# Performance work log

Hardware: AMD Instinct MI355X
Metric: run time of the kernel (lower is better)

## Reference

```python
import jax, jax.numpy as jnp
import numpy as np

HIDDEN = 256
HEADS = 8
HEAD_DIM = HIDDEN // HEADS  # 32
N_NODES = 50000
N_EDGES = 800000


def setup_inputs() -> dict:
    key = jax.random.key(0)
    ks = jax.random.split(key, 12)
    h = jax.random.normal(ks[0], (N_NODES, HIDDEN), dtype=jnp.float32)
    row = jax.random.randint(ks[1], (N_EDGES,), 0, N_NODES, dtype=jnp.int64 if jax.config.jax_enable_x64 else jnp.int32)
    col = jax.random.randint(ks[2], (N_EDGES,), 0, N_NODES, dtype=jnp.int64 if jax.config.jax_enable_x64 else jnp.int32)
    def lin(kw, kb):
        W = jax.random.normal(kw, (HIDDEN, HIDDEN), dtype=jnp.float32) * 0.02
        b = jax.random.normal(kb, (HIDDEN,), dtype=jnp.float32) * 0.02
        return W, b
    Wq, bq = lin(ks[3], ks[4])
    Wk, bk = lin(ks[5], ks[6])
    Wv, bv = lin(ks[7], ks[8])
    Wo, bo = lin(ks[9], ks[10])
    return {"h": h, "row": row, "col": col,
            "Wq": Wq, "bq": bq, "Wk": Wk, "bk": bk,
            "Wv": Wv, "bv": bv, "Wo": Wo, "bo": bo}


def reference(h, row, col, Wq, bq, Wk, bk, Wv, bv, Wo, bo):
    N = h.shape[0]
    scaling = HEAD_DIM ** (-0.5)
    # torch Linear: x @ W.T + b; reshape to (N, head_dim, num_heads) as in source
    q = (h @ Wq.T + bq).reshape(N, HEAD_DIM, HEADS) * scaling
    k = (h @ Wk.T + bk).reshape(N, HEAD_DIM, HEADS)
    v = (h @ Wv.T + bv).reshape(N, HEAD_DIM, HEADS)
    # SDDMM: per-edge, per-head score = q[row] . k[col]   -> [E, H]
    s = jnp.einsum('edh,edh->eh', q[row], k[col])
    # sparse softmax over nonzeros of each row
    m = jax.ops.segment_max(s, row, num_segments=N)          # [N, H]
    e = jnp.exp(s - m[row])                                   # [E, H]
    z = jax.ops.segment_sum(e, row, num_segments=N)          # [N, H]
    attn = e / z[row]                                         # [E, H]
    # SPMM: out[i] = sum over edges (i,j) attn[e,h] * v[j,:,h]
    out = jax.ops.segment_sum(attn[:, None, :] * v[col], row, num_segments=N)  # [N, D, H]
    return out.reshape(N, -1) @ Wo.T + bo
```

## Files before the change

### kernel.cpp

```cpp
#include <hip/hip_runtime.h>
#include <hip/hip_bf16.h>
#include <math.h>

#define N_NODES  50000
#define N_EDGES  800000
#define HIDDEN   256
#define HEADS    8
#define HEAD_DIM 32
#define MAXDEG   64
#define KVSTRIDE 512
#define MTILES   391

using short8 = __attribute__((ext_vector_type(8))) short;
using f32x4  = __attribute__((ext_vector_type(4))) float;

__device__ __forceinline__ float b2f(unsigned short u) {
  union { unsigned int i; float f; } v; v.i = ((unsigned int)u) << 16; return v.f;
}
__device__ __forceinline__ unsigned short f2b(float f) {
  union { float f; unsigned int i; } v; v.f = f;
  unsigned int r = v.i + 0x7FFF + ((v.i >> 16) & 1);
  return (unsigned short)(r >> 16);
}
__device__ __forceinline__ void unpack2(unsigned int d, float& lo, float& hi) {
  union { unsigned int i; float f; } a, b;
  a.i = d << 16; b.i = d & 0xFFFF0000u;
  lo = a.f; hi = b.f;
}

__global__ __launch_bounds__(256) void detect(const unsigned short* __restrict__ h16,
                                              const int* __restrict__ rowraw,
                                              int* __restrict__ flags) {
  __shared__ int nan_cnt, hi_viol, lo_pos;
  const int tid = threadIdx.x;
  if (tid == 0) { nan_cnt = 0; hi_viol = 0; lo_pos = 0; }
  __syncthreads();
  int local = 0;
  for (int i = tid; i < 16384; i += 256)
    if ((h16[i] & 0x7F80) == 0x7F80) local++;
  if (local) atomicAdd(&nan_cnt, local);
  int viol = 0, pos = 0;
  for (int e = tid; e < 512; e += 256) {
    if (rowraw[2 * e + 1] != 0) viol++;
    if (rowraw[2 * e] > 0) pos++;
  }
  if (viol) atomicAdd(&hi_viol, viol);
  if (pos) atomicAdd(&lo_pos, pos);
  __syncthreads();
  if (tid == 0) {
    flags[0] = (nan_cnt >= 4) ? 1 : 0;
    flags[1] = (hi_viol == 0 && lo_pos > 0) ? 1 : 0;
  }
}

__global__ __launch_bounds__(256) void conv_f4(const void* __restrict__ src,
                                               unsigned short* __restrict__ dst, int n4,
                                               const int* __restrict__ flags) {
  const int fp32 = flags[0];
  for (int i = blockIdx.x * 256 + threadIdx.x; i < n4; i += gridDim.x * 256) {
    if (fp32) {
      const float4 v = ((const float4*)src)[i];
      ushort4 o; o.x = f2b(v.x); o.y = f2b(v.y); o.z = f2b(v.z); o.w = f2b(v.w);
      ((ushort4*)dst)[i] = o;
    } else {
      ((ushort4*)dst)[i] = ((const ushort4*)src)[i];
    }
  }
}

struct WPtrs {
  const void* srcW[4]; unsigned short* dstW[4];
  const void* srcB[4]; unsigned short* dstB[4];
};
__global__ __launch_bounds__(256) void conv_wb(WPtrs p, const int* __restrict__ flags) {
  const int fp32 = flags[0];
  const int idx = blockIdx.x * 256 + threadIdx.x;
  if (idx < 49152) {
    const int m = idx >> 14, r = idx & 16383;
    const int g = r >> 6, kc = r & 63;
    const int f = ((g & 31) << 3) | (g >> 5);
    const int s = f * 64 + kc;
    if (fp32) {
      const float4 v = ((const float4*)p.srcW[m])[s];
      ushort4 o; o.x = f2b(v.x); o.y = f2b(v.y); o.z = f2b(v.z); o.w = f2b(v.w);
      ((ushort4*)p.dstW[m])[g * 64 + kc] = o;
    } else {
      ((ushort4*)p.dstW[m])[g * 64 + kc] = ((const ushort4*)p.srcW[m])[s];
    }
  } else if (idx < 49152 + 65536) {
    const int g = idx - 49152;
    const int f = g >> 8, kk = g & 255;
    const int s = f * 256 + (((kk & 31) << 3) | (kk >> 5));
    p.dstW[3][g] = fp32 ? f2b(((const float*)p.srcW[3])[s])
                        : ((const unsigned short*)p.srcW[3])[s];
  } else if (idx < 49152 + 65536 + 256) {
    const int t = idx - 49152 - 65536;
    const int m = t >> 6, r = t & 63;
    if (m < 3) {
      ushort4 o;
      #pragma unroll
      for (int x = 0; x < 4; ++x) {
        const int g = r * 4 + x;
        const int f = ((g & 31) << 3) | (g >> 5);
        ((unsigned short*)&o)[x] = fp32 ? f2b(((const float*)p.srcB[m])[f])
                                        : ((const unsigned short*)p.srcB[m])[f];
      }
      ((ushort4*)p.dstB[m])[r] = o;
    } else {
      if (fp32) {
        const float4 v = ((const float4*)p.srcB[3])[r];
        ushort4 o; o.x = f2b(v.x); o.y = f2b(v.y); o.z = f2b(v.z); o.w = f2b(v.w);
        ((ushort4*)p.dstB[3])[r] = o;
      } else {
        ((ushort4*)p.dstB[3])[r] = ((const ushort4*)p.srcB[3])[r];
      }
    }
  }
}

__global__ __launch_bounds__(256) void build_buckets(
    const int* __restrict__ rowraw, const int* __restrict__ colraw,
    const int* __restrict__ flags, int* __restrict__ cursor, int* __restrict__ bucket)
{
  const int e = blockIdx.x * 256 + threadIdx.x;
  if (e >= N_EDGES) return;
  const int i64 = flags[1];
  const int r = i64 ? rowraw[2 * e] : rowraw[e];
  const int c = i64 ? colraw[2 * e] : colraw[e];
  const int pos = atomicAdd(&cursor[r], 1);
  if (pos < MAXDEG) bucket[r * MAXDEG + pos] = c;
}

#if defined(__has_builtin)
#if __has_builtin(__builtin_amdgcn_global_load_lds)
#define HAVE_GLL 1
#endif
#endif
__device__ __forceinline__ void stage_tile(
    const unsigned short* __restrict__ src, int row_base, int row_max,
    int kb, unsigned short* lds, int wave, int lane)
{
  #pragma unroll
  for (int c = 0; c < 4; ++c) {
    const int chunk = wave * 4 + c;
    const int r = chunk * 8 + (lane >> 3);
    int gr = row_base + r; if (gr > row_max) gr = row_max;
    const int scb = (lane & 7) ^ ((lane >> 3) & 7);
    const unsigned short* gp = src + (size_t)gr * HIDDEN + kb * 64 + scb * 8;
#ifdef HAVE_GLL
    __builtin_amdgcn_global_load_lds(
        (const __attribute__((address_space(1))) void*)gp,
        (__attribute__((address_space(3))) void*)(lds + chunk * 512),
        16, 0, 0);
#else
    *(short8*)(lds + chunk * 512 + lane * 8) = *(const short8*)gp;
#endif
  }
}

#define GEMM_CORE(A_SRC, AROWB, AROWM, B_SRC, BROWB, BROWM)                          \
  __shared__ unsigned short sA[8192], sB[8192];                                      \
  const int wave = threadIdx.x >> 6, lane = threadIdx.x & 63;                        \
  const int lrow = lane & 15, quad = lane >> 4;                                      \
  const int wr0 = (wave & 1) * 64, wc0 = (wave >> 1) * 64;                           \
  f32x4 acc[4][4];                                                                   \
  _Pragma("unroll")                                                                  \
  for (int i = 0; i < 4; ++i)                                                        \
    _Pragma("unroll")                                                                \
    for (int j = 0; j < 4; ++j) acc[i][j] = (f32x4){0.f, 0.f, 0.f, 0.f};            \
  for (int kb = 0; kb < 4; ++kb) {                                                   \
    if (kb) __syncthreads();                                                         \
    stage_tile(A_SRC, AROWB, AROWM, kb, sA, wave, lane);                             \
    stage_tile(B_SRC, BROWB, BROWM, kb, sB, wave, lane);                             \
    __syncthreads();                                                                 \
    _Pragma("unroll")                                                                \
    for (int kk = 0; kk < 2; ++kk) {                                                 \
      short8 af[4], bf[4];                                                           \
      _Pragma("unroll")                                                              \
      for (int i = 0; i < 4; ++i) {                                                  \
        const int rr = wr0 + i * 16 + lrow;                                          \
        af[i] = *(const short8*)(sA + rr * 64 + (((kk * 4 + quad) ^ (lrow & 7)) * 8));\
      }                                                                              \
      _Pragma("unroll")                                                              \
      for (int j = 0; j < 4; ++j) {                                                  \
        const int rr = wc0 + j * 16 + lrow;                                          \
        bf[j] = *(const short8*)(sB + rr * 64 + (((kk * 4 + quad) ^ (lrow & 7)) * 8));\
      }                                                                              \
      _Pragma("unroll")                                                              \
      for (int i = 0; i < 4; ++i)                                                    \
        _Pragma("unroll")                                                            \
        for (int j = 0; j < 4; ++j)                                                  \
          acc[i][j] = __builtin_amdgcn_mfma_f32_16x16x32_bf16(af[i], bf[j], acc[i][j], 0, 0, 0); \
    }                                                                                \
  }

__global__ __launch_bounds__(256) void gemm_qkv(
    const unsigned short* __restrict__ X, const unsigned short* __restrict__ WQKV,
    const unsigned short* __restrict__ biasAll,
    unsigned short* __restrict__ Qt, unsigned short* __restrict__ KV, float qscale)
{
  const int row0 = blockIdx.x * 128;
  const int col0 = blockIdx.y * 128;
  GEMM_CORE(X, row0, N_NODES - 1, WQKV, col0, 767)

  #pragma unroll
  for (int j = 0; j < 4; ++j) {
    const int gcol = col0 + wc0 + j * 16;
    const int m = gcol >> 8;
    const int f = (gcol & 255) + lrow;
    const float scale = (m == 0) ? qscale : 1.0f;
    const float bv = b2f(biasAll[gcol + lrow]);
    unsigned short* bp = (m == 0) ? Qt : (KV + ((m == 2) ? 256 : 0));
    const int ldv = (m == 0) ? 256 : KVSTRIDE;
    #pragma unroll
    for (int i = 0; i < 4; ++i) {
      #pragma unroll
      for (int r = 0; r < 4; ++r) {
        const int row = row0 + wr0 + i * 16 + quad * 4 + r;
        if (row < N_NODES)
          bp[(size_t)row * ldv + f] = f2b((acc[i][j][r] + bv) * scale);
      }
    }
  }
}

__global__ __launch_bounds__(256) void gemm_o(
    const unsigned short* __restrict__ X, const unsigned short* __restrict__ W,
    const unsigned short* __restrict__ bias, void* __restrict__ Yv,
    const int* __restrict__ flags)
{
  const int row0 = blockIdx.x * 128;
  const int col0 = blockIdx.y * 128;
  const int out_fp32 = flags[0];
  GEMM_CORE(X, row0, N_NODES - 1, W, col0, 255)

  #pragma unroll
  for (int j = 0; j < 4; ++j) {
    const int col = col0 + wc0 + j * 16 + lrow;
    const float bv = b2f(bias[col]);
    #pragma unroll
    for (int i = 0; i < 4; ++i) {
      #pragma unroll
      for (int r = 0; r < 4; ++r) {
        const int row = row0 + wr0 + i * 16 + quad * 4 + r;
        if (row < N_NODES) {
          const float y = acc[i][j][r] + bv;
          if (out_fp32) ((float*)Yv)[(size_t)row * HIDDEN + col] = y;
          else ((unsigned short*)Yv)[(size_t)row * HIDDEN + col] = f2b(y);
        }
      }
    }
  }
}

__global__ __launch_bounds__(256) void attn_fused(
    const unsigned short* __restrict__ Qt, const unsigned short* __restrict__ KV,
    const int* __restrict__ cursor, const int* __restrict__ bucket,
    unsigned short* __restrict__ pre)
{
  const int node = blockIdx.x * 4 + (threadIdx.x >> 6);
  if (node >= N_NODES) return;
  const int lane = threadIdx.x & 63;
  const int side = lane >> 5;
  const int sub  = lane & 31;
  const unsigned suboff = (unsigned)(sub * 8);
  int cnt = cursor[node]; if (cnt > MAXDEG) cnt = MAXDEG;

  const uint4 qd = *(const uint4*)(Qt + (unsigned)node * HIDDEN + suboff);
  float q[8];
  unpack2(qd.x, q[0], q[1]); unpack2(qd.y, q[2], q[3]);
  unpack2(qd.z, q[4], q[5]); unpack2(qd.w, q[6], q[7]);

  float a[8] = {0.f, 0.f, 0.f, 0.f, 0.f, 0.f, 0.f, 0.f};
  float z = 0.f;

  if (cnt > 0) {
    const int last = cnt - 1;
    const int* brow = bucket + node * MAXDEG;
    const int myidx = brow[lane <= last ? lane : last];
    const int nit = (cnt + 1) >> 1;

    auto compute = [&](const uint4& kk, const uint4& vv, int jj) {
      float kf[8];
      unpack2(kk.x, kf[0], kf[1]); unpack2(kk.y, kf[2], kf[3]);
      unpack2(kk.z, kf[4], kf[5]); unpack2(kk.w, kf[6], kf[7]);
      float s0 = q[0]*kf[0] + q[2]*kf[2] + q[4]*kf[4] + q[6]*kf[6];
      float s1 = q[1]*kf[1] + q[3]*kf[3] + q[5]*kf[5] + q[7]*kf[7];
      float d = s0 + s1;
      d += __shfl_xor(d, 1, 64);
      d += __shfl_xor(d, 2, 64);
      float w = __expf(d);
      if (2 * jj + side > last) w = 0.f;
      z += w;
      float vf[8];
      unpack2(vv.x, vf[0], vf[1]); unpack2(vv.y, vf[2], vf[3]);
      unpack2(vv.z, vf[4], vf[5]); unpack2(vv.w, vf[6], vf[7]);
      #pragma unroll
      for (int x = 0; x < 8; ++x) a[x] = fmaf(w, vf[x], a[x]);
    };

    const int cA = __shfl(myidx, side, 64);
    const unsigned offA = ((unsigned)cA << 9) + suboff;
    uint4 kA = *(const uint4*)(KV + offA);
    uint4 vA = *(const uint4*)(KV + offA + 256u);

    const int cB = __shfl(myidx, 2 + side, 64);
    const unsigned offB = ((unsigned)cB << 9) + suboff;
    uint4 kB = *(const uint4*)(KV + offB);
    uint4 vB = *(const uint4*)(KV + offB + 256u);

    int slC = 4 + side;
    int cC = __shfl(myidx, slC, 64);

    int j = 0;
    #pragma unroll 2
    for (; j + 2 < nit; ++j) {
      const unsigned offC = ((unsigned)cC << 9) + suboff;
      const uint4 kC = *(const uint4*)(KV + offC);
      const uint4 vC = *(const uint4*)(KV + offC + 256u);
      int sl = 2 * (j + 3) + side; if (sl > 63) sl = 63;
      cC = __shfl(myidx, sl, 64);
      compute(kA, vA, j);
      kA = kB; vA = vB; kB = kC; vB = vC;
    }
    compute(kA, vA, j);
    if (j + 1 < nit) compute(kB, vB, j + 1);
  }

  #pragma unroll
  for (int x = 0; x < 8; ++x) a[x] += __shfl_xor(a[x], 32, 64);
  z += __shfl_xor(z, 32, 64);
  const float zi = (z > 0.f) ? (1.f / z) : 0.f;

  if (side == 0) {
    short8 ov;
    #pragma unroll
    for (int x = 0; x < 8; ++x) ov[x] = (short)f2b(a[x] * zi);
    *(short8*)(pre + (unsigned)node * HIDDEN + suboff) = ov;
  }
}

extern "C" void kernel_launch(void* const* d_in, const int* in_sizes, int n_in,
                              void* d_out, int out_size, void* d_ws, size_t ws_size,
                              hipStream_t stream) {
  const void* h_raw  = d_in[0];
  const int* row_raw = (const int*)d_in[1];
  const int* col_raw = (const int*)d_in[2];
  const void* Wq_raw = d_in[3]; const void* bq_raw = d_in[4];
  const void* Wk_raw = d_in[5]; const void* bk_raw = d_in[6];
  const void* Wv_raw = d_in[7]; const void* bv_raw = d_in[8];
  const void* Wo_raw = d_in[9]; const void* bo_raw = d_in[10];

  char* ws = (char*)d_ws;
  unsigned short* Qt   = (unsigned short*)(ws +          0);
  unsigned short* KV   = (unsigned short*)(ws +  25600000);
  int*            cur  = (int*)           (ws +  76800000);
  int*            bkt  = (int*)           (ws +  77000000);
  unsigned short* pre  = (unsigned short*)(ws +  89800000);
  unsigned short* WqP  = (unsigned short*)(ws + 115400000);
  unsigned short* WkP  = WqP + 65536;
  unsigned short* WvP  = WkP + 65536;
  unsigned short* WoP  = WvP + 65536;
  unsigned short* bqP  = (unsigned short*)(ws + 116000000);
  unsigned short* bkP  = bqP + 256;
  unsigned short* bvP  = bkP + 256;
  unsigned short* boC  = bvP + 256;
  int*            flags = (int*)(ws + 116100000);
  unsigned short* Hc   = (unsigned short*)(ws + 117000000);

  hipMemsetAsync(cur, 0, (size_t)N_NODES * 4, stream);

  detect<<<1, 256, 0, stream>>>((const unsigned short*)h_raw, row_raw, flags);

  conv_f4<<<6400, 256, 0, stream>>>(h_raw, Hc, N_NODES * HIDDEN / 4, flags);

  WPtrs wp;
  wp.srcW[0] = Wq_raw; wp.srcW[1] = Wk_raw; wp.srcW[2] = Wv_raw; wp.srcW[3] = Wo_raw;
  wp.dstW[0] = WqP;    wp.dstW[1] = WkP;    wp.dstW[2] = WvP;    wp.dstW[3] = WoP;
  wp.srcB[0] = bq_raw; wp.srcB[1] = bk_raw; wp.srcB[2] = bv_raw; wp.srcB[3] = bo_raw;
  wp.dstB[0] = bqP;    wp.dstB[1] = bkP;    wp.dstB[2] = bvP;    wp.dstB[3] = boC;
  conv_wb<<<(114944 + 255) / 256, 256, 0, stream>>>(wp, flags);

  build_buckets<<<(N_EDGES + 255) / 256, 256, 0, stream>>>(row_raw, col_raw, flags, cur, bkt);

  dim3 qgrid(MTILES, 6);
  gemm_qkv<<<qgrid, 256, 0, stream>>>(Hc, WqP, bqP, Qt, KV, 0.17677669529663687f);

  attn_fused<<<(N_NODES + 3) / 4, 256, 0, stream>>>(Qt, KV, cur, bkt, pre);

  dim3 ogrid(MTILES, 2);
  gemm_o<<<ogrid, 256, 0, stream>>>(pre, WoP, boC, d_out, flags);
}
```

Measured before the change: 393.4 us.

## Merge prep kernels, remap GEMM blocks per XCD, store bucket indices as u16

Merges the memset, detect, h conversion, weight conversion and bucket build into two launches (init and prep), which cuts launch count and inter-kernel gaps. Bucket column indices are stored as 16-bit values, halving bucket traffic in attn_fused. GEMM grids are flattened and remapped so consecutive tiles land on the same XCD, aiming for better L2 reuse of weight and activation tiles. The 16-bit indices assume node ids fit in 16 bits, but N_NODES is 50000, which still fits within 65535.

```diff
diff --git a/kernel.cpp b/kernel.cpp
--- a/kernel.cpp
+++ b/kernel.cpp
@@ -9,7 +9,8 @@
 #define HEAD_DIM 32
 #define MAXDEG   64
 #define KVSTRIDE 512
-#define MTILES   391
+#define QKV_NB   2346
+#define O_NB     782
 
 using short8 = __attribute__((ext_vector_type(8))) short;
 using f32x4  = __attribute__((ext_vector_type(4))) float;
@@ -28,43 +29,42 @@
   lo = a.f; hi = b.f;
 }
 
-__global__ __launch_bounds__(256) void detect(const unsigned short* __restrict__ h16,
-                                              const int* __restrict__ rowraw,
-                                              int* __restrict__ flags) {
-  __shared__ int nan_cnt, hi_viol, lo_pos;
+template<int NB, int NCT>
+__device__ __forceinline__ void xcd_map(int b, int& rt, int& ct) {
+  constexpr int q = NB / 8, r = NB % 8;
+  const int xcd = b & 7, j = b >> 3;
+  const int id = (xcd < r ? xcd * (q + 1) : r * (q + 1) + (xcd - r) * q) + j;
+  rt = id / NCT; ct = id - rt * NCT;
+}
+
+__global__ __launch_bounds__(256) void init(const unsigned short* __restrict__ h16,
+                                            const int* __restrict__ rowraw,
+                                            int* __restrict__ flags,
+                                            int* __restrict__ cur) {
   const int tid = threadIdx.x;
-  if (tid == 0) { nan_cnt = 0; hi_viol = 0; lo_pos = 0; }
-  __syncthreads();
-  int local = 0;
-  for (int i = tid; i < 16384; i += 256)
-    if ((h16[i] & 0x7F80) == 0x7F80) local++;
-  if (local) atomicAdd(&nan_cnt, local);
-  int viol = 0, pos = 0;
-  for (int e = tid; e < 512; e += 256) {
-    if (rowraw[2 * e + 1] != 0) viol++;
-    if (rowraw[2 * e] > 0) pos++;
-  }
-  if (viol) atomicAdd(&hi_viol, viol);
-  if (pos) atomicAdd(&lo_pos, pos);
-  __syncthreads();
-  if (tid == 0) {
-    flags[0] = (nan_cnt >= 4) ? 1 : 0;
-    flags[1] = (hi_viol == 0 && lo_pos > 0) ? 1 : 0;
-  }
-}
-
-__global__ __launch_bounds__(256) void conv_f4(const void* __restrict__ src,
-                                               unsigned short* __restrict__ dst, int n4,
-                                               const int* __restrict__ flags) {
-  const int fp32 = flags[0];
-  for (int i = blockIdx.x * 256 + threadIdx.x; i < n4; i += gridDim.x * 256) {
-    if (fp32) {
-      const float4 v = ((const float4*)src)[i];
-      ushort4 o; o.x = f2b(v.x); o.y = f2b(v.y); o.z = f2b(v.z); o.w = f2b(v.w);
-      ((ushort4*)dst)[i] = o;
-    } else {
-      ((ushort4*)dst)[i] = ((const ushort4*)src)[i];
-    }
+  if (blockIdx.x == 0) {
+    __shared__ int nan_cnt, hi_viol, lo_pos;
+    if (tid == 0) { nan_cnt = 0; hi_viol = 0; lo_pos = 0; }
+    __syncthreads();
+    int local = 0;
+    for (int i = tid; i < 16384; i += 256)
+      if ((h16[i] & 0x7F80) == 0x7F80) local++;
+    if (local) atomicAdd(&nan_cnt, local);
+    int viol = 0, pos = 0;
+    for (int e = tid; e < 512; e += 256) {
+      if (rowraw[2 * e + 1] != 0) viol++;
+      if (rowraw[2 * e] > 0) pos++;
+    }
+    if (viol) atomicAdd(&hi_viol, viol);
+    if (pos) atomicAdd(&lo_pos, pos);
+    __syncthreads();
+    if (tid == 0) {
+      flags[0] = (nan_cnt >= 4) ? 1 : 0;
+      flags[1] = (hi_viol == 0 && lo_pos > 0) ? 1 : 0;
+    }
+  } else {
+    const int i = (blockIdx.x - 1) * 256 + tid;
+    if (i < N_NODES / 4) ((int4*)cur)[i] = make_int4(0, 0, 0, 0);
   }
 }
 
@@ -72,63 +72,80 @@
   const void* srcW[4]; unsigned short* dstW[4];
   const void* srcB[4]; unsigned short* dstB[4];
 };
-__global__ __launch_bounds__(256) void conv_wb(WPtrs p, const int* __restrict__ flags) {
+
+__global__ __launch_bounds__(256) void prep(
+    const void* __restrict__ hsrc, unsigned short* __restrict__ Hc, WPtrs p,
+    const int* __restrict__ rowraw, const int* __restrict__ colraw,
+    const int* __restrict__ flags, int* __restrict__ cursor,
+    unsigned short* __restrict__ bucket)
+{
   const int fp32 = flags[0];
-  const int idx = blockIdx.x * 256 + threadIdx.x;
-  if (idx < 49152) {
-    const int m = idx >> 14, r = idx & 16383;
-    const int g = r >> 6, kc = r & 63;
-    const int f = ((g & 31) << 3) | (g >> 5);
-    const int s = f * 64 + kc;
-    if (fp32) {
-      const float4 v = ((const float4*)p.srcW[m])[s];
-      ushort4 o; o.x = f2b(v.x); o.y = f2b(v.y); o.z = f2b(v.z); o.w = f2b(v.w);
-      ((ushort4*)p.dstW[m])[g * 64 + kc] = o;
-    } else {
-      ((ushort4*)p.dstW[m])[g * 64 + kc] = ((const ushort4*)p.srcW[m])[s];
-    }
-  } else if (idx < 49152 + 65536) {
-    const int g = idx - 49152;
-    const int f = g >> 8, kk = g & 255;
-    const int s = f * 256 + (((kk & 31) << 3) | (kk >> 5));
-    p.dstW[3][g] = fp32 ? f2b(((const float*)p.srcW[3])[s])
-                        : ((const unsigned short*)p.srcW[3])[s];
-  } else if (idx < 49152 + 65536 + 256) {
-    const int t = idx - 49152 - 65536;
-    const int m = t >> 6, r = t & 63;
-    if (m < 3) {
-      ushort4 o;
-      #pragma unroll
-      for (int x = 0; x < 4; ++x) {
-        const int g = r * 4 + x;
-        const int f = ((g & 31) << 3) | (g >> 5);
-        ((unsigned short*)&o)[x] = fp32 ? f2b(((const float*)p.srcB[m])[f])
-                                        : ((const unsigned short*)p.srcB[m])[f];
+  const int bid = blockIdx.x, tid = threadIdx.x;
+
+  if (bid < 6400) {
+    const int n4 = N_NODES * HIDDEN / 4;
+    for (int i = bid * 256 + tid; i < n4; i += 6400 * 256) {
+      if (fp32) {
+        const float4 v = ((const float4*)hsrc)[i];
+        ushort4 o; o.x = f2b(v.x); o.y = f2b(v.y); o.z = f2b(v.z); o.w = f2b(v.w);
+        ((ushort4*)Hc)[i] = o;
+      } else {
+        ((ushort4*)Hc)[i] = ((const ushort4*)hsrc)[i];
       }
-      ((ushort4*)p.dstB[m])[r] = o;
-    } else {
+    }
+  } else if (bid < 6850) {
+    const int idx = (bid - 6400) * 256 + tid;
+    if (idx < 49152) {
+      const int m = idx >> 14, r = idx & 16383;
+      const int g = r >> 6, kc = r & 63;
+      const int f = ((g & 31) << 3) | (g >> 5);
+      const int s = f * 64 + kc;
       if (fp32) {
-        const float4 v = ((const float4*)p.srcB[3])[r];
+        const float4 v = ((const float4*)p.srcW[m])[s];
         ushort4 o; o.x = f2b(v.x); o.y = f2b(v.y); o.z = f2b(v.z); o.w = f2b(v.w);
-        ((ushort4*)p.dstB[3])[r] = o;
+        ((ushort4*)p.dstW[m])[g * 64 + kc] = o;
       } else {
-        ((ushort4*)p.dstB[3])[r] = ((const ushort4*)p.srcB[3])[r];
+        ((ushort4*)p.dstW[m])[g * 64 + kc] = ((const ushort4*)p.srcW[m])[s];
       }
-    }
-  }
-}
-
-__global__ __launch_bounds__(256) void build_buckets(
-    const int* __restrict__ rowraw, const int* __restrict__ colraw,
-    const int* __restrict__ flags, int* __restrict__ cursor, int* __restrict__ bucket)
-{
-  const int e = blockIdx.x * 256 + threadIdx.x;
-  if (e >= N_EDGES) return;
-  const int i64 = flags[1];
-  const int r = i64 ? rowraw[2 * e] : rowraw[e];
-  const int c = i64 ? colraw[2 * e] : colraw[e];
-  const int pos = atomicAdd(&cursor[r], 1);
-  if (pos < MAXDEG) bucket[r * MAXDEG + pos] = c;
+    } else if (idx < 49152 + 65536) {
+      const int g = idx - 49152;
+      const int f = g >> 8, kk = g & 255;
+      const int s = f * 256 + (((kk & 31) << 3) | (kk >> 5));
+      p.dstW[3][g] = fp32 ? f2b(((const float*)p.srcW[3])[s])
+                          : ((const unsigned short*)p.srcW[3])[s];
+    } else if (idx < 49152 + 65536 + 256) {
+      const int t = idx - 49152 - 65536;
+      const int m = t >> 6, r = t & 63;
+      if (m < 3) {
+        ushort4 o;
+        #pragma unroll
+        for (int x = 0; x < 4; ++x) {
+          const int g = r * 4 + x;
+          const int f = ((g & 31) << 3) | (g >> 5);
+          ((unsigned short*)&o)[x] = fp32 ? f2b(((const float*)p.srcB[m])[f])
+                                          : ((const unsigned short*)p.srcB[m])[f];
+        }
+        ((ushort4*)p.dstB[m])[r] = o;
+      } else {
+        if (fp32) {
+          const float4 v = ((const float4*)p.srcB[3])[r];
+          ushort4 o; o.x = f2b(v.x); o.y = f2b(v.y); o.z = f2b(v.z); o.w = f2b(v.w);
+          ((ushort4*)p.dstB[3])[r] = o;
+        } else {
+          ((ushort4*)p.dstB[3])[r] = ((const ushort4*)p.srcB[3])[r];
+        }
+      }
+    }
+  } else {
+    const int e = (bid - 6850) * 256 + tid;
+    if (e < N_EDGES) {
+      const int i64 = flags[1];
+      const int r = i64 ? rowraw[2 * e] : rowraw[e];
+      const int c = i64 ? colraw[2 * e] : colraw[e];
+      const int pos = atomicAdd(&cursor[r], 1);
+      if (pos < MAXDEG) bucket[r * MAXDEG + pos] = (unsigned short)c;
+    }
+  }
 }
 
 #if defined(__has_builtin)
@@ -199,8 +216,9 @@
     const unsigned short* __restrict__ biasAll,
     unsigned short* __restrict__ Qt, unsigned short* __restrict__ KV, float qscale)
 {
-  const int row0 = blockIdx.x * 128;
-  const int col0 = blockIdx.y * 128;
+  int rt, ct; xcd_map<QKV_NB, 6>(blockIdx.x, rt, ct);
+  const int row0 = rt * 128;
+  const int col0 = ct * 128;
   GEMM_CORE(X, row0, N_NODES - 1, WQKV, col0, 767)
 
   #pragma unroll
@@ -229,8 +247,9 @@
     const unsigned short* __restrict__ bias, void* __restrict__ Yv,
     const int* __restrict__ flags)
 {
-  const int row0 = blockIdx.x * 128;
-  const int col0 = blockIdx.y * 128;
+  int rt, ct; xcd_map<O_NB, 2>(blockIdx.x, rt, ct);
+  const int row0 = rt * 128;
+  const int col0 = ct * 128;
   const int out_fp32 = flags[0];
   GEMM_CORE(X, row0, N_NODES - 1, W, col0, 255)
 
@@ -255,7 +274,7 @@
 
 __global__ __launch_bounds__(256) void attn_fused(
     const unsigned short* __restrict__ Qt, const unsigned short* __restrict__ KV,
-    const int* __restrict__ cursor, const int* __restrict__ bucket,
+    const int* __restrict__ cursor, const unsigned short* __restrict__ bucket,
     unsigned short* __restrict__ pre)
 {
   const int node = blockIdx.x * 4 + (threadIdx.x >> 6);
@@ -276,8 +295,8 @@
 
   if (cnt > 0) {
     const int last = cnt - 1;
-    const int* brow = bucket + node * MAXDEG;
-    const int myidx = brow[lane <= last ? lane : last];
+    const unsigned short* brow = bucket + node * MAXDEG;
+    const int myidx = (int)brow[lane <= last ? lane : last];
     const int nit = (cnt + 1) >> 1;
 
     auto compute = [&](const uint4& kk, const uint4& vv, int jj) {
@@ -355,7 +374,7 @@
   unsigned short* Qt   = (unsigned short*)(ws +          0);
   unsigned short* KV   = (unsigned short*)(ws +  25600000);
   int*            cur  = (int*)           (ws +  76800000);
-  int*            bkt  = (int*)           (ws +  77000000);
+  unsigned short* bkt  = (unsigned short*)(ws +  77000000);
   unsigned short* pre  = (unsigned short*)(ws +  89800000);
   unsigned short* WqP  = (unsigned short*)(ws + 115400000);
   unsigned short* WkP  = WqP + 65536;
@@ -368,26 +387,18 @@
   int*            flags = (int*)(ws + 116100000);
   unsigned short* Hc   = (unsigned short*)(ws + 117000000);
 
-  hipMemsetAsync(cur, 0, (size_t)N_NODES * 4, stream);
-
-  detect<<<1, 256, 0, stream>>>((const unsigned short*)h_raw, row_raw, flags);
-
-  conv_f4<<<6400, 256, 0, stream>>>(h_raw, Hc, N_NODES * HIDDEN / 4, flags);
+  init<<<64, 256, 0, stream>>>((const unsigned short*)h_raw, row_raw, flags, cur);
 
   WPtrs wp;
   wp.srcW[0] = Wq_raw; wp.srcW[1] = Wk_raw; wp.srcW[2] = Wv_raw; wp.srcW[3] = Wo_raw;
   wp.dstW[0] = WqP;    wp.dstW[1] = WkP;    wp.dstW[2] = WvP;    wp.dstW[3] = WoP;
   wp.srcB[0] = bq_raw; wp.srcB[1] = bk_raw; wp.srcB[2] = bv_raw; wp.srcB[3] = bo_raw;
   wp.dstB[0] = bqP;    wp.dstB[1] = bkP;    wp.dstB[2] = bvP;    wp.dstB[3] = boC;
-  conv_wb<<<(114944 + 255) / 256, 256, 0, stream>>>(wp, flags);
-
-  build_buckets<<<(N_EDGES + 255) / 256, 256, 0, stream>>>(row_raw, col_raw, flags, cur, bkt);
-
-  dim3 qgrid(MTILES, 6);
-  gemm_qkv<<<qgrid, 256, 0, stream>>>(Hc, WqP, bqP, Qt, KV, 0.17677669529663687f);
+  prep<<<9975, 256, 0, stream>>>(h_raw, Hc, wp, row_raw, col_raw, flags, cur, bkt);
+
+  gemm_qkv<<<QKV_NB, 256, 0, stream>>>(Hc, WqP, bqP, Qt, KV, 0.17677669529663687f);
 
   attn_fused<<<(N_NODES + 3) / 4, 256, 0, stream>>>(Qt, KV, cur, bkt, pre);
 
-  dim3 ogrid(MTILES, 2);
-  gemm_o<<<ogrid, 256, 0, stream>>>(pre, WoP, boC, d_out, flags);
-}
+  gemm_o<<<O_NB, 256, 0, stream>>>(pre, WoP, boC, d_out, flags);
+}
```

Result: faster. 383.7 us (-2.5%).
